# Performance work log

Hardware: AMD Instinct MI355X
Metric: run time of the kernel (lower is better)

The kernel has to match this reference:

```python
import jax, jax.numpy as jnp
import numpy as np

EPS = 1e-5
HEADS = 16
D_HEAD = 64
SCALE = D_HEAD ** -0.5


def layernorm(x, g, b):
    m = jnp.mean(x, axis=-1, keepdims=True)
    v = jnp.var(x, axis=-1, keepdims=True)
    return (x - m) * jax.lax.rsqrt(v + EPS) * g + b


def attention(x, ctx, Wq, Wk, Wv, Wo, bo):
    b, n, _ = x.shape
    m = ctx.shape[1]
    q = (x @ Wq).reshape(b, n, HEADS, D_HEAD)
    k = (ctx @ Wk).reshape(b, m, HEADS, D_HEAD)
    v = (ctx @ Wv).reshape(b, m, HEADS, D_HEAD)
    sim = jnp.einsum('bihd,bjhd->bhij', q, k) * SCALE  # [b,h,n,m]
    attn = jax.nn.softmax(sim, axis=-1)
    out = jnp.einsum('bhij,bjhd->bihd', attn, v).reshape(b, n, HEADS * D_HEAD)
    return out @ Wo + bo


def setup_inputs() -> dict:
    key = jax.random.key(0)
    ks = jax.random.split(key, 16)
    dim, ctx_dim, inner = 1024, 768, HEADS * D_HEAD
    ff_inner = 4 * dim
    s = lambda k, *sh: jax.random.normal(k, sh, jnp.float32) * 0.02
    return {
        'x': jax.random.normal(ks[0], (2, 2048, dim), jnp.float32),
        'context': jax.random.normal(ks[1], (2, 77, ctx_dim), jnp.float32),
        'ln1_g': jnp.ones((dim,), jnp.float32), 'ln1_b': jnp.zeros((dim,), jnp.float32),
        'a1_Wq': s(ks[2], dim, inner), 'a1_Wk': s(ks[3], dim, inner), 'a1_Wv': s(ks[4], dim, inner),
        'a1_Wo': s(ks[5], inner, dim), 'a1_bo': jnp.zeros((dim,), jnp.float32),
        'ln2_g': jnp.ones((dim,), jnp.float32), 'ln2_b': jnp.zeros((dim,), jnp.float32),
        'a2_Wq': s(ks[6], dim, inner), 'a2_Wk': s(ks[7], ctx_dim, inner), 'a2_Wv': s(ks[8], ctx_dim, inner),
        'a2_Wo': s(ks[9], inner, dim), 'a2_bo': jnp.zeros((dim,), jnp.float32),
        'ln3_g': jnp.ones((dim,), jnp.float32), 'ln3_b': jnp.zeros((dim,), jnp.float32),
        'ff_Wp': s(ks[10], dim, 2 * ff_inner), 'ff_bp': jnp.zeros((2 * ff_inner,), jnp.float32),
        'ff_Wo': s(ks[11], ff_inner, dim), 'ff_bo': jnp.zeros((dim,), jnp.float32),
    }


def reference(x, context, ln1_g, ln1_b, a1_Wq, a1_Wk, a1_Wv, a1_Wo, a1_bo,
              ln2_g, ln2_b, a2_Wq, a2_Wk, a2_Wv, a2_Wo, a2_bo,
              ln3_g, ln3_b, ff_Wp, ff_bp, ff_Wo, ff_bo):
    h = layernorm(x, ln1_g, ln1_b)
    x = attention(h, h, a1_Wq, a1_Wk, a1_Wv, a1_Wo, a1_bo) + x
    h = layernorm(x, ln2_g, ln2_b)
    x = attention(h, context, a2_Wq, a2_Wk, a2_Wv, a2_Wo, a2_bo) + x
    h = layernorm(x, ln3_g, ln3_b)
    p = h @ ff_Wp + ff_bp
    u, gate = jnp.split(p, 2, axis=-1)
    ff = (u * jax.nn.gelu(gate, approximate=False)) @ ff_Wo + ff_bo
    return ff + x
```

## Files before the change

### kernel.cpp

```cpp
#include <hip/hip_runtime.h>
#include <hip/hip_bf16.h>

typedef __hip_bfloat16 bf16;
typedef short s16x8 __attribute__((ext_vector_type(8)));
typedef float f32x4 __attribute__((ext_vector_type(4)));

#define NSEQ 2048
#define DIM  1024
#define CTXD 768
#define INNER 1024
#define NH 16
#define DH 64
#define NB 2
#define TOK (NB*NSEQ)
#define MCTX 77
#define CTOK (NB*MCTX)
#define VSTR_X 128

__device__ __forceinline__ void gload_lds16(const void* g, void* lds) {
  __builtin_amdgcn_global_load_lds(
      (const __attribute__((address_space(1))) unsigned int*)g,
      (__attribute__((address_space(3))) unsigned int*)lds, 16, 0, 0);
}

template<int REMAP>
__global__ __launch_bounds__(256)
void wt_transpose(const float* __restrict__ W, bf16* __restrict__ WT, int K, int N) {
  __shared__ float tile[32][33];
  const int r = threadIdx.x >> 5, c = threadIdx.x & 31;
  const int k0 = blockIdx.x * 32, n0 = blockIdx.y * 32;
#pragma unroll
  for (int i = 0; i < 4; ++i)
    tile[r + i*8][c] = W[(size_t)(k0 + r + i*8) * N + n0 + c];
  __syncthreads();
#pragma unroll
  for (int i = 0; i < 4; ++i) {
    int n = n0 + r + i*8;
    if (REMAP) n = (n < (N >> 1)) ? 2*n : 2*(n - (N >> 1)) + 1;
    WT[(size_t)n * K + k0 + c] = __float2bfloat16(tile[c][r + i*8]);
  }
}

__global__ __launch_bounds__(256)
void cvt_bf16_kernel(const float* __restrict__ in, bf16* __restrict__ out, int n) {
  int i = blockIdx.x * 256 + threadIdx.x;
  if (i < n) out[i] = __float2bfloat16(in[i]);
}

__global__ __launch_bounds__(256)
void bias_inter_kernel(const float* __restrict__ bp, float* __restrict__ bpi) {
  int i = blockIdx.x * 256 + threadIdx.x;
  int n = (i < 4096) ? 2*i : 2*(i - 4096) + 1;
  bpi[n] = bp[i];
}

__global__ __launch_bounds__(256)
void zero_kernel(float4* __restrict__ p, int n16) {
  int i = blockIdx.x * 256 + threadIdx.x;
  if (i < n16) p[i] = make_float4(0.f, 0.f, 0.f, 0.f);
}

__global__ __launch_bounds__(256)
void ln_kernel(const float* __restrict__ x, const float* __restrict__ gw,
               const float* __restrict__ bw, bf16* __restrict__ out) {
  const int row = blockIdx.x;
  const int t = threadIdx.x;
  const float4 xv = ((const float4*)(x + (size_t)row * DIM))[t];
  float s = xv.x + xv.y + xv.z + xv.w;
  float q = xv.x*xv.x + xv.y*xv.y + xv.z*xv.z + xv.w*xv.w;
#pragma unroll
  for (int m = 1; m < 64; m <<= 1) { s += __shfl_xor(s, m); q += __shfl_xor(q, m); }
  __shared__ float red[8];
  const int lane = t & 63, w = t >> 6;
  if (lane == 0) { red[w] = s; red[4 + w] = q; }
  __syncthreads();
  s = red[0] + red[1] + red[2] + red[3];
  q = red[4] + red[5] + red[6] + red[7];
  const float mean = s * (1.f / DIM);
  const float var = q * (1.f / DIM) - mean * mean;
  const float rs = rsqrtf(var + 1e-5f);
  const float4 gv = ((const float4*)gw)[t];
  const float4 bv = ((const float4*)bw)[t];
  union { bf16 h[4]; uint2 u; } o;
  o.h[0] = __float2bfloat16((xv.x - mean) * rs * gv.x + bv.x);
  o.h[1] = __float2bfloat16((xv.y - mean) * rs * gv.y + bv.y);
  o.h[2] = __float2bfloat16((xv.z - mean) * rs * gv.z + bv.z);
  o.h[3] = __float2bfloat16((xv.w - mean) * rs * gv.w + bv.w);
  ((uint2*)(out + (size_t)row * DIM))[t] = o.u;
}

template<int EPI, int BN>
__global__ __launch_bounds__(256)
void gemm_bt(const bf16* __restrict__ A, const bf16* __restrict__ Bt,
             void* __restrict__ o0, void* __restrict__ o1, void* __restrict__ o2,
             const float* __restrict__ bias, const float* __restrict__ resid,
             int M, int Nn, int K, float scale) {
  constexpr int NT = BN / 32;
  __shared__ bf16 Als[128 * 64];
  __shared__ bf16 Bls[BN * 64];
  const int tid = threadIdx.x;
  const int lane = tid & 63;
  const int w = tid >> 6;
  const int g = lane >> 4, r16 = lane & 15;
  const int tm = blockIdx.x * 128, tn = blockIdx.y * BN;
  const int wm = (w >> 1) * 64, wn = (w & 1) * (BN / 2);

  f32x4 acc[4][NT];
#pragma unroll
  for (int i = 0; i < 4; ++i)
#pragma unroll
    for (int j = 0; j < NT; ++j) acc[i][j] = (f32x4){0.f, 0.f, 0.f, 0.f};

  for (int kt = 0; kt < K; kt += 64) {
    __syncthreads();
#pragma unroll
    for (int i = 0; i < 4; ++i) {
      const int slot = (w * 4 + i) * 64 + lane;
      const int row = slot >> 3;
      const int sch = (slot & 7) ^ (row & 7);
      int ar = tm + row; ar = ar < M ? ar : M - 1;
      gload_lds16(A + (size_t)ar * K + kt + sch * 8, (char*)Als + (w * 4 + i) * 1024);
    }
#pragma unroll
    for (int i = 0; i < NT; ++i) {
      const int slot = (w * NT + i) * 64 + lane;
      const int row = slot >> 3;
      const int sch = (slot & 7) ^ (row & 7);
      gload_lds16(Bt + (size_t)(tn + row) * K + kt + sch * 8, (char*)Bls + (w * NT + i) * 1024);
    }
    __syncthreads();
#pragma unroll
    for (int kk = 0; kk < 2; ++kk) {
      s16x8 af[4], bfr[NT];
#pragma unroll
      for (int mt = 0; mt < 4; ++mt) {
        const int row = wm + mt * 16 + r16;
        const int ch = (kk * 4 + g) ^ (row & 7);
        af[mt] = *(const s16x8*)((const char*)Als + row * 128 + ch * 16);
      }
#pragma unroll
      for (int nt = 0; nt < NT; ++nt) {
        const int row = wn + nt * 16 + r16;
        const int ch = (kk * 4 + g) ^ (row & 7);
        bfr[nt] = *(const s16x8*)((const char*)Bls + row * 128 + ch * 16);
      }
#pragma unroll
      for (int mt = 0; mt < 4; ++mt)
#pragma unroll
        for (int nt = 0; nt < NT; ++nt)
          acc[mt][nt] = __builtin_amdgcn_mfma_f32_16x16x32_bf16(af[mt], bfr[nt], acc[mt][nt], 0, 0, 0);
    }
  }

#pragma unroll
  for (int mt = 0; mt < 4; ++mt) {
    const int row0 = tm + wm + mt * 16 + 4 * g;
#pragma unroll
    for (int nt = 0; nt < NT; ++nt) {
      const int col = tn + wn + nt * 16 + r16;
#pragma unroll
      for (int j = 0; j < 4; ++j) {
        const int row = row0 + j;
        const float v = acc[mt][nt][j];
        if (EPI == 4) {
          const float val = v + bias[col];
          const float oth = __shfl_xor(val, 1);
          if (row < M && (r16 & 1) == 0) {
            const float ge = 0.5f * oth * (1.f + erff(oth * 0.70710678118654752f));
            ((bf16*)o0)[(size_t)row * (Nn >> 1) + (col >> 1)] = __float2bfloat16(val * ge);
          }
          continue;
        }
        if (row >= M) continue;
        if (EPI == 0) {
          ((bf16*)o0)[(size_t)row * Nn + col] = __float2bfloat16(v * scale);
        } else if (EPI == 2) {
          ((float*)o0)[(size_t)row * Nn + col] = v + bias[col] + resid[(size_t)row * Nn + col];
        } else if (EPI == 5) {
          const int seg = tn >> 10;
          const int lcol = col - (seg << 10);
          if (seg == 0) {
            ((bf16*)o0)[(size_t)row * INNER + lcol] = __float2bfloat16(v * 0.125f);
          } else if (seg == 1) {
            ((bf16*)o1)[(size_t)row * INNER + lcol] = __float2bfloat16(v);
          } else {
            const int b = row >> 11, i = row & (NSEQ - 1);
            ((bf16*)o2)[((size_t)(b * INNER + lcol)) * NSEQ + i] = __float2bfloat16(v);
          }
        } else if (EPI == 6) {
          const int seg = tn >> 10;
          const int lcol = col - (seg << 10);
          if (seg == 0) {
            ((bf16*)o0)[(size_t)row * INNER + lcol] = __float2bfloat16(v);
          } else {
            const int b = row / MCTX, i = row - b * MCTX;
            ((bf16*)o2)[((size_t)(b * INNER + lcol)) * VSTR_X + i] = __float2bfloat16(v);
          }
        }
      }
    }
  }
}

__global__ __launch_bounds__(256)
void attn_kernel(const bf16* __restrict__ q, const bf16* __restrict__ k,
                 const bf16* __restrict__ vT, bf16* __restrict__ out,
                 int m_kv, int vstr) {
  __shared__ bf16 Kls[64 * 64];
  __shared__ bf16 Vls[80 * 64];
  __shared__ bf16 Pls[4][32 * 64];

  const int tid = threadIdx.x, lane = tid & 63, w = tid >> 6;
  const int g = lane >> 4, r16 = lane & 15;
  const int qt = blockIdx.x, h = blockIdx.y, b = blockIdx.z;

  s16x8 qf[2][2];
#pragma unroll
  for (int mt = 0; mt < 2; ++mt) {
    const int qrow = qt * 128 + w * 32 + mt * 16 + r16;
    const bf16* qb_ = q + ((size_t)(b * NSEQ + qrow)) * INNER + h * DH;
    qf[mt][0] = *(const s16x8*)(qb_ + 8 * g);
    qf[mt][1] = *(const s16x8*)(qb_ + 32 + 8 * g);
  }

  {
    const unsigned int ones2 = 0x3F803F80u;
    uint2 val;
    val.x = (tid < 16) ? ones2 : 0u;
    val.y = val.x;
    *(uint2*)((char*)Vls + 64 * 128 + tid * 8) = val;
  }

  f32x4 acc[2][5];
#pragma unroll
  for (int mt = 0; mt < 2; ++mt)
#pragma unroll
    for (int nt = 0; nt < 5; ++nt) acc[mt][nt] = (f32x4){0.f, 0.f, 0.f, 0.f};

  const int ntiles = (m_kv + 63) >> 6;
  int4 kreg[2], vreg[2];

  auto prefetch = [&](int kt) {
#pragma unroll
    for (int i = 0; i < 2; ++i) {
      const int slot = i * 256 + tid;
      const int row = slot >> 3;
      const int sch = (slot & 7) ^ (row & 7);
      const int key = kt * 64 + row;
      kreg[i] = (key < m_kv)
          ? *(const int4*)(k + ((size_t)(b * m_kv + key)) * INNER + h * DH + sch * 8)
          : (int4){0, 0, 0, 0};
      vreg[i] = *(const int4*)(vT + ((size_t)(b * INNER + h * DH + row)) * vstr + kt * 64 + sch * 8);
    }
  };

  prefetch(0);
  bf16* pw = &Pls[w][0];

  for (int kt = 0; kt < ntiles; ++kt) {
    const bool full = (kt * 64 + 64) <= m_kv;
    __syncthreads();
#pragma unroll
    for (int i = 0; i < 2; ++i) {
      const int slot = i * 256 + tid;
      *(int4*)((char*)Kls + slot * 16) = kreg[i];
      *(int4*)((char*)Vls + slot * 16) = vreg[i];
    }
    __syncthreads();
    if (kt + 1 < ntiles) prefetch(kt + 1);

    f32x4 s4[2][4];
#pragma unroll
    for (int mt = 0; mt < 2; ++mt)
#pragma unroll
      for (int nt = 0; nt < 4; ++nt) s4[mt][nt] = (f32x4){0.f, 0.f, 0.f, 0.f};
#pragma unroll
    for (int kk = 0; kk < 2; ++kk) {
      s16x8 kf[4];
#pragma unroll
      for (int nt = 0; nt < 4; ++nt) {
        const int row = nt * 16 + r16;
        const int ch = (kk * 4 + g) ^ (row & 7);
        kf[nt] = *(const s16x8*)((const char*)Kls + row * 128 + ch * 16);
      }
#pragma unroll
      for (int mt = 0; mt < 2; ++mt)
#pragma unroll
        for (int nt = 0; nt < 4; ++nt)
          s4[mt][nt] = __builtin_amdgcn_mfma_f32_16x16x32_bf16(qf[mt][kk], kf[nt], s4[mt][nt], 0, 0, 0);
    }
    if (!full) {
#pragma unroll
      for (int nt = 0; nt < 4; ++nt) {
        const int key = kt * 64 + nt * 16 + r16;
        if (key >= m_kv) {
#pragma unroll
          for (int mt = 0; mt < 2; ++mt) {
            s4[mt][nt][0] = -1e30f; s4[mt][nt][1] = -1e30f;
            s4[mt][nt][2] = -1e30f; s4[mt][nt][3] = -1e30f;
          }
        }
      }
    }

#pragma unroll
    for (int mt = 0; mt < 2; ++mt) {
#pragma unroll
      for (int j = 0; j < 4; ++j) {
        const int prow = mt * 16 + 4 * g + j;
        const int rowbase = prow * 128;
        const int sw = (prow & 7) << 4;
#pragma unroll
        for (int nt = 0; nt < 4; ++nt) {
          const float p = __expf(s4[mt][nt][j]);
          const int byte = rowbase + ((nt * 32 + r16 * 2) ^ sw);
          *(bf16*)((char*)pw + byte) = __float2bfloat16(p);
        }
      }
    }

#pragma unroll
    for (int kk = 0; kk < 2; ++kk) {
      s16x8 vf[5];
#pragma unroll
      for (int nt = 0; nt < 5; ++nt) {
        const int row = nt * 16 + r16;
        const int ch = (kk * 4 + g) ^ (row & 7);
        vf[nt] = *(const s16x8*)((const char*)Vls + row * 128 + ch * 16);
      }
#pragma unroll
      for (int mt = 0; mt < 2; ++mt) {
        const int prow = mt * 16 + r16;
        const int pch = (kk * 4 + g) ^ (prow & 7);
        const s16x8 pa = *(const s16x8*)((const char*)pw + prow * 128 + pch * 16);
#pragma unroll
        for (int nt = 0; nt < 5; ++nt)
          acc[mt][nt] = __builtin_amdgcn_mfma_f32_16x16x32_bf16(pa, vf[nt], acc[mt][nt], 0, 0, 0);
      }
    }
  }

#pragma unroll
  for (int mt = 0; mt < 2; ++mt) {
#pragma unroll
    for (int j = 0; j < 4; ++j) {
      const float rs = 1.f / __shfl(acc[mt][4][j], lane & 48);
      const int row = qt * 128 + w * 32 + mt * 16 + 4 * g + j;
#pragma unroll
      for (int nt = 0; nt < 4; ++nt) {
        const int col = h * DH + nt * 16 + r16;
        out[((size_t)(b * NSEQ + row)) * INNER + col] = __float2bfloat16(acc[mt][nt][j] * rs);
      }
    }
  }
}

extern "C" void kernel_launch(void* const* d_in, const int* in_sizes, int n_in,
                              void* d_out, int out_size, void* d_ws, size_t ws_size,
                              hipStream_t stream) {
  const float* x    = (const float*)d_in[0];
  const float* ctx  = (const float*)d_in[1];
  const float* ln1g = (const float*)d_in[2];
  const float* ln1b = (const float*)d_in[3];
  const float* Wq1  = (const float*)d_in[4];
  const float* Wk1  = (const float*)d_in[5];
  const float* Wv1  = (const float*)d_in[6];
  const float* Wo1  = (const float*)d_in[7];
  const float* bo1  = (const float*)d_in[8];
  const float* ln2g = (const float*)d_in[9];
  const float* ln2b = (const float*)d_in[10];
  const float* Wq2  = (const float*)d_in[11];
  const float* Wk2  = (const float*)d_in[12];
  const float* Wv2  = (const float*)d_in[13];
  const float* Wo2  = (const float*)d_in[14];
  const float* bo2  = (const float*)d_in[15];
  const float* ln3g = (const float*)d_in[16];
  const float* ln3b = (const float*)d_in[17];
  const float* Wp   = (const float*)d_in[18];
  const float* bp   = (const float*)d_in[19];
  const float* Wf   = (const float*)d_in[20];
  const float* bfo  = (const float*)d_in[21];

  char* ws = (char*)d_ws;
  size_t off = 0;
  auto alloc = [&](size_t bytes) { char* p = ws + off; off += (bytes + 255) & ~(size_t)255; return p; };
  bf16* wqkvT = (bf16*)alloc((size_t)3072 * 1024 * 2);
  bf16* wo1T  = (bf16*)alloc((size_t)1024 * 1024 * 2);
  bf16* wq2T  = (bf16*)alloc((size_t)1024 * 1024 * 2);
  bf16* wkv2T = (bf16*)alloc((size_t)2048 * 768 * 2);
  bf16* wo2T  = (bf16*)alloc((size_t)1024 * 1024 * 2);
  bf16* wpT   = (bf16*)alloc((size_t)8192 * 1024 * 2);
  bf16* wfT   = (bf16*)alloc((size_t)1024 * 4096 * 2);
  float* bpi  = (float*)alloc((size_t)8192 * 4);
  bf16* ctxb  = (bf16*)alloc((size_t)CTOK * CTXD * 2);
  bf16* hb    = (bf16*)alloc((size_t)TOK * DIM * 2);
  bf16* qb    = (bf16*)alloc((size_t)TOK * INNER * 2);
  bf16* kb    = (bf16*)alloc((size_t)TOK * INNER * 2);
  bf16* vTb   = (bf16*)alloc((size_t)NB * INNER * NSEQ * 2);
  bf16* ao    = (bf16*)alloc((size_t)TOK * INNER * 2);
  float* xbuf = (float*)alloc((size_t)TOK * DIM * 4);
  bf16* ffin  = (bf16*)alloc((size_t)TOK * 4096 * 2);

  const dim3 blk(256);
  wt_transpose<0><<<dim3(32, 32), blk, 0, stream>>>(Wq1, wqkvT, 1024, 1024);
  wt_transpose<0><<<dim3(32, 32), blk, 0, stream>>>(Wk1, wqkvT + (size_t)1024 * 1024, 1024, 1024);
  wt_transpose<0><<<dim3(32, 32), blk, 0, stream>>>(Wv1, wqkvT + (size_t)2048 * 1024, 1024, 1024);
  wt_transpose<0><<<dim3(32, 32), blk, 0, stream>>>(Wo1, wo1T, 1024, 1024);
  wt_transpose<0><<<dim3(32, 32), blk, 0, stream>>>(Wq2, wq2T, 1024, 1024);
  wt_transpose<0><<<dim3(24, 32), blk, 0, stream>>>(Wk2, wkv2T, 768, 1024);
  wt_transpose<0><<<dim3(24, 32), blk, 0, stream>>>(Wv2, wkv2T + (size_t)1024 * 768, 768, 1024);
  wt_transpose<0><<<dim3(32, 32), blk, 0, stream>>>(Wo2, wo2T, 1024, 1024);
  wt_transpose<1><<<dim3(32, 256), blk, 0, stream>>>(Wp, wpT, 1024, 8192);
  wt_transpose<0><<<dim3(128, 32), blk, 0, stream>>>(Wf, wfT, 4096, 1024);
  bias_inter_kernel<<<dim3(32), blk, 0, stream>>>(bp, bpi);
  cvt_bf16_kernel<<<dim3((CTOK * CTXD + 255) / 256), blk, 0, stream>>>(ctx, ctxb, CTOK * CTXD);

  ln_kernel<<<dim3(TOK), blk, 0, stream>>>(x, ln1g, ln1b, hb);
  gemm_bt<5, 128><<<dim3(32, 24), blk, 0, stream>>>(hb, wqkvT, qb, kb, vTb, nullptr, nullptr, TOK, 3072, 1024, 1.f);
  attn_kernel<<<dim3(16, 16, 2), blk, 0, stream>>>(qb, kb, vTb, ao, NSEQ, NSEQ);
  gemm_bt<2, 64><<<dim3(32, 16), blk, 0, stream>>>(ao, wo1T, xbuf, nullptr, nullptr, bo1, x, TOK, 1024, 1024, 1.f);

  ln_kernel<<<dim3(TOK), blk, 0, stream>>>(xbuf, ln2g, ln2b, hb);
  gemm_bt<0, 64><<<dim3(32, 16), blk, 0, stream>>>(hb, wq2T, qb, nullptr, nullptr, nullptr, nullptr, TOK, 1024, 1024, 0.125f);
  zero_kernel<<<dim3((NB * INNER * VSTR_X * 2 / 16 + 255) / 256), blk, 0, stream>>>((float4*)vTb, NB * INNER * VSTR_X * 2 / 16);
  gemm_bt<6, 64><<<dim3(2, 32), blk, 0, stream>>>(ctxb, wkv2T, kb, nullptr, vTb, nullptr, nullptr, CTOK, 2048, 768, 1.f);
  attn_kernel<<<dim3(16, 16, 2), blk, 0, stream>>>(qb, kb, vTb, ao, MCTX, VSTR_X);
  gemm_bt<2, 64><<<dim3(32, 16), blk, 0, stream>>>(ao, wo2T, xbuf, nullptr, nullptr, bo2, xbuf, TOK, 1024, 1024, 1.f);

  ln_kernel<<<dim3(TOK), blk, 0, stream>>>(xbuf, ln3g, ln3b, hb);
  gemm_bt<4, 128><<<dim3(32, 64), blk, 0, stream>>>(hb, wpT, ffin, nullptr, nullptr, bpi, nullptr, TOK, 8192, 1024, 1.f);
  gemm_bt<2, 64><<<dim3(32, 16), blk, 0, stream>>>(ffin, wfT, (float*)d_out, nullptr, nullptr, bfo, xbuf, TOK, 1024, 4096, 1.f);

  (void)in_sizes; (void)n_in; (void)out_size; (void)ws_size;
}
```

Baseline: 578.5 us.

## Merge prep kernels into one launch and block-interleave GEGLU weight columns

Replaces the ten weight-transpose launches, bias interleave, context conversion and zero kernel with one prep_kernel that dispatches on block index. It also gives the cross-attention V its own buffer so the zeroing can move into the prep launch. The GEGLU weight and bias layout changes from per-column interleave to 32-column blocks, so each thread holds u and gate in separate accumulator tiles. This removes the shuffle and the half-idle lanes in the GEGLU epilogue. The cost is a larger branchy prep kernel and an epilogue that assumes the fixed block layout and drops its row bounds check.

Result: faster. 538.8 us (-6.9%).

```diff
diff --git a/kernel.cpp b/kernel.cpp
--- a/kernel.cpp
+++ b/kernel.cpp
@@ -23,12 +23,12 @@
       (__attribute__((address_space(3))) unsigned int*)lds, 16, 0, 0);
 }
 
-template<int REMAP>
-__global__ __launch_bounds__(256)
-void wt_transpose(const float* __restrict__ W, bf16* __restrict__ WT, int K, int N) {
-  __shared__ float tile[32][33];
+__device__ __forceinline__ void wtile(float (*tile)[33], const float* __restrict__ W,
+                                      bf16* __restrict__ WT, int K, int N, int t, int REMAP) {
+  const int nkx = K >> 5;
+  const int kx = t % nkx, ny = t / nkx;
   const int r = threadIdx.x >> 5, c = threadIdx.x & 31;
-  const int k0 = blockIdx.x * 32, n0 = blockIdx.y * 32;
+  const int k0 = kx * 32, n0 = ny * 32;
 #pragma unroll
   for (int i = 0; i < 4; ++i)
     tile[r + i*8][c] = W[(size_t)(k0 + r + i*8) * N + n0 + c];
@@ -36,28 +36,61 @@
 #pragma unroll
   for (int i = 0; i < 4; ++i) {
     int n = n0 + r + i*8;
-    if (REMAP) n = (n < (N >> 1)) ? 2*n : 2*(n - (N >> 1)) + 1;
+    if (REMAP == 2) {
+      const int f = (n < 4096) ? n : n - 4096;
+      n = ((f >> 5) << 6) + ((n < 4096) ? 0 : 32) + (f & 31);
+    }
     WT[(size_t)n * K + k0 + c] = __float2bfloat16(tile[c][r + i*8]);
   }
 }
 
+#define PB1  1024
+#define PB2  2048
+#define PB3  3072
+#define PB4  4096
+#define PB5  5120
+#define PB6  5888
+#define PB7  6656
+#define PB8  7680
+#define PB9  15872
+#define PB10 19968
+#define PB11 20430
+#define PB12 20462
+#define PTOT 20590
+
 __global__ __launch_bounds__(256)
-void cvt_bf16_kernel(const float* __restrict__ in, bf16* __restrict__ out, int n) {
-  int i = blockIdx.x * 256 + threadIdx.x;
-  if (i < n) out[i] = __float2bfloat16(in[i]);
-}
-
-__global__ __launch_bounds__(256)
-void bias_inter_kernel(const float* __restrict__ bp, float* __restrict__ bpi) {
-  int i = blockIdx.x * 256 + threadIdx.x;
-  int n = (i < 4096) ? 2*i : 2*(i - 4096) + 1;
-  bpi[n] = bp[i];
-}
-
-__global__ __launch_bounds__(256)
-void zero_kernel(float4* __restrict__ p, int n16) {
-  int i = blockIdx.x * 256 + threadIdx.x;
-  if (i < n16) p[i] = make_float4(0.f, 0.f, 0.f, 0.f);
+void prep_kernel(const float* __restrict__ Wq1, const float* __restrict__ Wk1,
+                 const float* __restrict__ Wv1, const float* __restrict__ Wo1,
+                 const float* __restrict__ Wq2, const float* __restrict__ Wk2,
+                 const float* __restrict__ Wv2, const float* __restrict__ Wo2,
+                 const float* __restrict__ Wp,  const float* __restrict__ Wf,
+                 const float* __restrict__ bp,  const float* __restrict__ ctx,
+                 bf16* wqkvT, bf16* wo1T, bf16* wq2T, bf16* wkv2T, bf16* wo2T,
+                 bf16* wpT, bf16* wfT, float* bpi, bf16* ctxb, float4* vz) {
+  __shared__ float tile[32][33];
+  const int bid = blockIdx.x;
+  if (bid < PB1)        wtile(tile, Wq1, wqkvT,                         1024, 1024, bid,        0);
+  else if (bid < PB2)   wtile(tile, Wk1, wqkvT + (size_t)1024 * 1024,   1024, 1024, bid - PB1,  0);
+  else if (bid < PB3)   wtile(tile, Wv1, wqkvT + (size_t)2048 * 1024,   1024, 1024, bid - PB2,  0);
+  else if (bid < PB4)   wtile(tile, Wo1, wo1T,                          1024, 1024, bid - PB3,  0);
+  else if (bid < PB5)   wtile(tile, Wq2, wq2T,                          1024, 1024, bid - PB4,  0);
+  else if (bid < PB6)   wtile(tile, Wk2, wkv2T,                          768, 1024, bid - PB5,  0);
+  else if (bid < PB7)   wtile(tile, Wv2, wkv2T + (size_t)1024 * 768,     768, 1024, bid - PB6,  0);
+  else if (bid < PB8)   wtile(tile, Wo2, wo2T,                          1024, 1024, bid - PB7,  0);
+  else if (bid < PB9)   wtile(tile, Wp,  wpT,                           1024, 8192, bid - PB8,  2);
+  else if (bid < PB10)  wtile(tile, Wf,  wfT,                           4096, 1024, bid - PB9,  0);
+  else if (bid < PB11) {
+    const int i = (bid - PB10) * 256 + threadIdx.x;
+    ctxb[i] = __float2bfloat16(ctx[i]);
+  } else if (bid < PB12) {
+    const int i = (bid - PB11) * 256 + threadIdx.x;
+    const int f = (i < 4096) ? i : i - 4096;
+    const int n = ((f >> 5) << 6) + ((i < 4096) ? 0 : 32) + (f & 31);
+    bpi[n] = bp[i];
+  } else {
+    const int i = (bid - PB12) * 256 + threadIdx.x;
+    vz[i] = make_float4(0.f, 0.f, 0.f, 0.f);
+  }
 }
 
 __global__ __launch_bounds__(256)
@@ -152,49 +185,62 @@
     }
   }
 
-#pragma unroll
-  for (int mt = 0; mt < 4; ++mt) {
-    const int row0 = tm + wm + mt * 16 + 4 * g;
-#pragma unroll
-    for (int nt = 0; nt < NT; ++nt) {
-      const int col = tn + wn + nt * 16 + r16;
-#pragma unroll
-      for (int j = 0; j < 4; ++j) {
-        const int row = row0 + j;
-        const float v = acc[mt][nt][j];
-        if (EPI == 4) {
-          const float val = v + bias[col];
-          const float oth = __shfl_xor(val, 1);
-          if (row < M && (r16 & 1) == 0) {
-            const float ge = 0.5f * oth * (1.f + erff(oth * 0.70710678118654752f));
-            ((bf16*)o0)[(size_t)row * (Nn >> 1) + (col >> 1)] = __float2bfloat16(val * ge);
-          }
-          continue;
+  if constexpr (EPI == 4) {
+    const int base = tn + wn;
+#pragma unroll
+    for (int nt = 0; nt < 2; ++nt) {
+      const int cu = base + nt * 16 + r16;
+      const float bu = bias[cu];
+      const float bg = bias[cu + 32];
+      const int f = (base >> 1) + nt * 16 + r16;
+#pragma unroll
+      for (int mt = 0; mt < 4; ++mt) {
+        const int row0 = tm + wm + mt * 16 + 4 * g;
+#pragma unroll
+        for (int j = 0; j < 4; ++j) {
+          const float u  = acc[mt][nt][j] + bu;
+          const float gg = acc[mt][nt + 2][j] + bg;
+          const float ge = 0.5f * gg * (1.f + erff(gg * 0.70710678118654752f));
+          ((bf16*)o0)[(size_t)(row0 + j) * (Nn >> 1) + f] = __float2bfloat16(u * ge);
         }
-        if (row >= M) continue;
-        if (EPI == 0) {
-          ((bf16*)o0)[(size_t)row * Nn + col] = __float2bfloat16(v * scale);
-        } else if (EPI == 2) {
-          ((float*)o0)[(size_t)row * Nn + col] = v + bias[col] + resid[(size_t)row * Nn + col];
-        } else if (EPI == 5) {
-          const int seg = tn >> 10;
-          const int lcol = col - (seg << 10);
-          if (seg == 0) {
-            ((bf16*)o0)[(size_t)row * INNER + lcol] = __float2bfloat16(v * 0.125f);
-          } else if (seg == 1) {
-            ((bf16*)o1)[(size_t)row * INNER + lcol] = __float2bfloat16(v);
-          } else {
-            const int b = row >> 11, i = row & (NSEQ - 1);
-            ((bf16*)o2)[((size_t)(b * INNER + lcol)) * NSEQ + i] = __float2bfloat16(v);
-          }
-        } else if (EPI == 6) {
-          const int seg = tn >> 10;
-          const int lcol = col - (seg << 10);
-          if (seg == 0) {
-            ((bf16*)o0)[(size_t)row * INNER + lcol] = __float2bfloat16(v);
-          } else {
-            const int b = row / MCTX, i = row - b * MCTX;
-            ((bf16*)o2)[((size_t)(b * INNER + lcol)) * VSTR_X + i] = __float2bfloat16(v);
+      }
+    }
+  } else {
+#pragma unroll
+    for (int mt = 0; mt < 4; ++mt) {
+      const int row0 = tm + wm + mt * 16 + 4 * g;
+#pragma unroll
+      for (int nt = 0; nt < NT; ++nt) {
+        const int col = tn + wn + nt * 16 + r16;
+#pragma unroll
+        for (int j = 0; j < 4; ++j) {
+          const int row = row0 + j;
+          if (row >= M) continue;
+          const float v = acc[mt][nt][j];
+          if (EPI == 0) {
+            ((bf16*)o0)[(size_t)row * Nn + col] = __float2bfloat16(v * scale);
+          } else if (EPI == 2) {
+            ((float*)o0)[(size_t)row * Nn + col] = v + bias[col] + resid[(size_t)row * Nn + col];
+          } else if (EPI == 5) {
+            const int seg = tn >> 10;
+            const int lcol = col - (seg << 10);
+            if (seg == 0) {
+              ((bf16*)o0)[(size_t)row * INNER + lcol] = __float2bfloat16(v * 0.125f);
+            } else if (seg == 1) {
+              ((bf16*)o1)[(size_t)row * INNER + lcol] = __float2bfloat16(v);
+            } else {
+              const int b = row >> 11, i = row & (NSEQ - 1);
+              ((bf16*)o2)[((size_t)(b * INNER + lcol)) * NSEQ + i] = __float2bfloat16(v);
+            }
+          } else if (EPI == 6) {
+            const int seg = tn >> 10;
+            const int lcol = col - (seg << 10);
+            if (seg == 0) {
+              ((bf16*)o0)[(size_t)row * INNER + lcol] = __float2bfloat16(v);
+            } else {
+              const int b = row / MCTX, i = row - b * MCTX;
+              ((bf16*)o2)[((size_t)(b * INNER + lcol)) * VSTR_X + i] = __float2bfloat16(v);
+            }
           }
         }
       }
@@ -397,23 +443,16 @@
   bf16* qb    = (bf16*)alloc((size_t)TOK * INNER * 2);
   bf16* kb    = (bf16*)alloc((size_t)TOK * INNER * 2);
   bf16* vTb   = (bf16*)alloc((size_t)NB * INNER * NSEQ * 2);
+  bf16* vTb2  = (bf16*)alloc((size_t)NB * INNER * VSTR_X * 2);
   bf16* ao    = (bf16*)alloc((size_t)TOK * INNER * 2);
   float* xbuf = (float*)alloc((size_t)TOK * DIM * 4);
   bf16* ffin  = (bf16*)alloc((size_t)TOK * 4096 * 2);
 
   const dim3 blk(256);
-  wt_transpose<0><<<dim3(32, 32), blk, 0, stream>>>(Wq1, wqkvT, 1024, 1024);
-  wt_transpose<0><<<dim3(32, 32), blk, 0, stream>>>(Wk1, wqkvT + (size_t)1024 * 1024, 1024, 1024);
-  wt_transpose<0><<<dim3(32, 32), blk, 0, stream>>>(Wv1, wqkvT + (size_t)2048 * 1024, 1024, 1024);
-  wt_transpose<0><<<dim3(32, 32), blk, 0, stream>>>(Wo1, wo1T, 1024, 1024);
-  wt_transpose<0><<<dim3(32, 32), blk, 0, stream>>>(Wq2, wq2T, 1024, 1024);
-  wt_transpose<0><<<dim3(24, 32), blk, 0, stream>>>(Wk2, wkv2T, 768, 1024);
-  wt_transpose<0><<<dim3(24, 32), blk, 0, stream>>>(Wv2, wkv2T + (size_t)1024 * 768, 768, 1024);
-  wt_transpose<0><<<dim3(32, 32), blk, 0, stream>>>(Wo2, wo2T, 1024, 1024);
-  wt_transpose<1><<<dim3(32, 256), blk, 0, stream>>>(Wp, wpT, 1024, 8192);
-  wt_transpose<0><<<dim3(128, 32), blk, 0, stream>>>(Wf, wfT, 4096, 1024);
-  bias_inter_kernel<<<dim3(32), blk, 0, stream>>>(bp, bpi);
-  cvt_bf16_kernel<<<dim3((CTOK * CTXD + 255) / 256), blk, 0, stream>>>(ctx, ctxb, CTOK * CTXD);
+  prep_kernel<<<dim3(PTOT), blk, 0, stream>>>(Wq1, Wk1, Wv1, Wo1, Wq2, Wk2, Wv2, Wo2,
+                                              Wp, Wf, bp, ctx,
+                                              wqkvT, wo1T, wq2T, wkv2T, wo2T,
+                                              wpT, wfT, bpi, ctxb, (float4*)vTb2);
 
   ln_kernel<<<dim3(TOK), blk, 0, stream>>>(x, ln1g, ln1b, hb);
   gemm_bt<5, 128><<<dim3(32, 24), blk, 0, stream>>>(hb, wqkvT, qb, kb, vTb, nullptr, nullptr, TOK, 3072, 1024, 1.f);
@@ -422,9 +461,8 @@
 
   ln_kernel<<<dim3(TOK), blk, 0, stream>>>(xbuf, ln2g, ln2b, hb);
   gemm_bt<0, 64><<<dim3(32, 16), blk, 0, stream>>>(hb, wq2T, qb, nullptr, nullptr, nullptr, nullptr, TOK, 1024, 1024, 0.125f);
-  zero_kernel<<<dim3((NB * INNER * VSTR_X * 2 / 16 + 255) / 256), blk, 0, stream>>>((float4*)vTb, NB * INNER * VSTR_X * 2 / 16);
-  gemm_bt<6, 64><<<dim3(2, 32), blk, 0, stream>>>(ctxb, wkv2T, kb, nullptr, vTb, nullptr, nullptr, CTOK, 2048, 768, 1.f);
-  attn_kernel<<<dim3(16, 16, 2), blk, 0, stream>>>(qb, kb, vTb, ao, MCTX, VSTR_X);
+  gemm_bt<6, 64><<<dim3(2, 32), blk, 0, stream>>>(ctxb, wkv2T, kb, nullptr, vTb2, nullptr, nullptr, CTOK, 2048, 768, 1.f);
+  attn_kernel<<<dim3(16, 16, 2), blk, 0, stream>>>(qb, kb, vTb2, ao, MCTX, VSTR_X);
   gemm_bt<2, 64><<<dim3(32, 16), blk, 0, stream>>>(ao, wo2T, xbuf, nullptr, nullptr, bo2, xbuf, TOK, 1024, 1024, 1.f);
 
   ln_kernel<<<dim3(TOK), blk, 0, stream>>>(xbuf, ln3g, ln3b, hb);
```
